# Kernel tuning notes

Measured on AMD Instinct MI355X. Metric: run time of the kernel, lower is better.

The kernel has to match this reference:

```python
import jax, jax.numpy as jnp
import numpy as np

EMBED = 1024
HEADS = 16
INTERNAL = 1024  # embedding_dim // downsample_rate
HEAD_DIM = INTERNAL // HEADS


def setup_inputs() -> dict:
    key = jax.random.key(0)
    ks = jax.random.split(key, 12)
    B, S = 2, 2048
    s_in = 1.0 / np.sqrt(EMBED)
    s_out = 1.0 / np.sqrt(INTERNAL)
    return {
        "queries": jax.random.normal(ks[0], (B, S, EMBED), jnp.float32),
        "keys": jax.random.normal(ks[1], (B, S, EMBED), jnp.float32),
        "values": jax.random.normal(ks[2], (B, S, EMBED), jnp.float32),
        "Wq": jax.random.uniform(ks[3], (EMBED, INTERNAL), jnp.float32, -s_in, s_in),
        "bq": jax.random.uniform(ks[4], (INTERNAL,), jnp.float32, -s_in, s_in),
        "Wk": jax.random.uniform(ks[5], (EMBED, INTERNAL), jnp.float32, -s_in, s_in),
        "bk": jax.random.uniform(ks[6], (INTERNAL,), jnp.float32, -s_in, s_in),
        "Wv": jax.random.uniform(ks[7], (EMBED, INTERNAL), jnp.float32, -s_in, s_in),
        "bv": jax.random.uniform(ks[8], (INTERNAL,), jnp.float32, -s_in, s_in),
        "Wo": jax.random.uniform(ks[9], (INTERNAL, EMBED), jnp.float32, -s_out, s_out),
        "bo": jax.random.uniform(ks[10], (EMBED,), jnp.float32, -s_out, s_out),
    }


def _split_heads(x):
    B, S, D = x.shape
    return x.reshape(B, S, HEADS, D // HEADS).transpose(0, 2, 1, 3)  # bhsd


def reference(queries, keys, values, Wq, bq, Wk, bk, Wv, bv, Wo, bo):
    q = _split_heads(queries @ Wq + bq)
    k = _split_heads(keys @ Wk + bk)
    v = _split_heads(values @ Wv + bv)
    # NOTE: original scales by 1/sqrt(internal_dim), not 1/sqrt(head_dim)
    scale = 1.0 / np.sqrt(INTERNAL).astype(np.float32)
    scores = jnp.einsum("bhqd,bhkd->bhqk", q, k) * scale
    probs = jax.nn.softmax(scores, axis=-1)
    out = jnp.einsum("bhqk,bhkd->bhqd", probs, v)
    B, H, S, Dh = out.shape
    out = out.transpose(0, 2, 1, 3).reshape(B, S, H * Dh)
    return out @ Wo + bo
```

## Files before the change

kernel.cpp:

```cpp
#include <hip/hip_runtime.h>
#include <stdint.h>

typedef unsigned short u16;
typedef __attribute__((ext_vector_type(8))) short short8;
typedef __attribute__((ext_vector_type(4))) float f32x4;
typedef __attribute__((ext_vector_type(16))) float f32x16;
typedef __attribute__((ext_vector_type(8))) unsigned short u16x8;
typedef __attribute__((ext_vector_type(4))) unsigned short u16x4;
typedef __attribute__((ext_vector_type(4))) uint32_t u32x4;

#if __has_builtin(__builtin_amdgcn_exp2f)
#define EXP2(x) __builtin_amdgcn_exp2f(x)
#else
#define EXP2(x) exp2f(x)
#endif

__device__ __forceinline__ u16 f2bf(float f) {
  union { float f; uint32_t u; } v; v.f = f;
  uint32_t r = (v.u + 0x7FFFu + ((v.u >> 16) & 1u)) >> 16;
  return (u16)r;
}

__device__ __forceinline__ uint32_t pack2(float a, float b) {
  return (__float_as_uint(b) & 0xffff0000u) | (__float_as_uint(a) >> 16);
}

__device__ __forceinline__ void gload_lds16(const void* g, void* l) {
  __builtin_amdgcn_global_load_lds(
      (const __attribute__((address_space(1))) void*)g,
      (__attribute__((address_space(3))) void*)l,
      16, 0, 0);
}

__global__ __launch_bounds__(256) void cvt_x(const float* __restrict__ q,
                                             const float* __restrict__ k,
                                             const float* __restrict__ v,
                                             u16* __restrict__ dst) {
  const float* src = blockIdx.z == 0 ? q : (blockIdx.z == 1 ? k : v);
  u16* d = dst + (size_t)blockIdx.z * (4096u * 1024u);
  size_t i = ((size_t)blockIdx.x * 256 + threadIdx.x) * 8;
  float4 a = *(const float4*)(src + i);
  float4 b = *(const float4*)(src + i + 4);
  u16x8 o;
  o[0] = f2bf(a.x); o[1] = f2bf(a.y); o[2] = f2bf(a.z); o[3] = f2bf(a.w);
  o[4] = f2bf(b.x); o[5] = f2bf(b.y); o[6] = f2bf(b.z); o[7] = f2bf(b.w);
  *(u16x8*)(d + i) = o;
}

__global__ __launch_bounds__(256) void cvt_wt(const float* __restrict__ Wq,
                                              const float* __restrict__ Wk,
                                              const float* __restrict__ Wv,
                                              const float* __restrict__ Wo,
                                              u16* __restrict__ Wt4) {
  const float* W = blockIdx.z == 0 ? Wq : (blockIdx.z == 1 ? Wk
                   : (blockIdx.z == 2 ? Wv : Wo));
  u16* Wt = Wt4 + (size_t)blockIdx.z * (1024u * 1024u);
  __shared__ u16 tile[64][65];
  int kt = blockIdx.x * 64, nt = blockIdx.y * 64;
  int t = threadIdx.x;
#pragma unroll
  for (int r = 0; r < 4; ++r) {
    int id = t + r * 256;
    int kk = id >> 4, c4 = id & 15;
    float4 vv = *(const float4*)(W + (size_t)(kt + kk) * 1024 + nt + c4 * 4);
    tile[kk][c4 * 4 + 0] = f2bf(vv.x);
    tile[kk][c4 * 4 + 1] = f2bf(vv.y);
    tile[kk][c4 * 4 + 2] = f2bf(vv.z);
    tile[kk][c4 * 4 + 3] = f2bf(vv.w);
  }
  __syncthreads();
#pragma unroll
  for (int r = 0; r < 4; ++r) {
    int id = t + r * 256;
    int n = id >> 4, kc = id & 15;
    u16x4 o;
    o[0] = tile[kc * 4 + 0][n];
    o[1] = tile[kc * 4 + 1][n];
    o[2] = tile[kc * 4 + 2][n];
    o[3] = tile[kc * 4 + 3][n];
    *(u16x4*)(Wt + (size_t)(nt + n) * 1024 + kt + kc * 4) = o;
  }
}

template <bool F32OUT>
__device__ __forceinline__ void gemm_tile(const u16* __restrict__ A,
                                          const u16* __restrict__ Bt,
                                          const float* __restrict__ bias,
                                          u16* __restrict__ Cb,
                                          float* __restrict__ Cf,
                                          float scale, int bm, int bn) {
  __shared__ u16 Alds[128 * 64];
  __shared__ u16 Blds[128 * 64];
  const int tid = threadIdx.x;
  const int lane = tid & 63, w = tid >> 6;
  const int wm = (w >> 1) * 64, wn = (w & 1) * 64;
  const int l15 = lane & 15, lg = lane >> 4;

  f32x4 acc[4][4] = {};

  int srow[4], scol[4], soff[4];
#pragma unroll
  for (int i = 0; i < 4; ++i) {
    int o = (w * 4 + i) * 1024 + lane * 16;
    int row = o >> 7;
    int kc = ((o >> 4) & 7) ^ (row & 7);
    srow[i] = row; scol[i] = kc * 8; soff[i] = o;
  }

  for (int kt = 0; kt < 16; ++kt) {
    __syncthreads();
#pragma unroll
    for (int i = 0; i < 4; ++i) {
      gload_lds16(A + (size_t)(bm * 128 + srow[i]) * 1024 + kt * 64 + scol[i],
                  (char*)Alds + soff[i]);
      gload_lds16(Bt + (size_t)(bn * 128 + srow[i]) * 1024 + kt * 64 + scol[i],
                  (char*)Blds + soff[i]);
    }
    __syncthreads();
#pragma unroll
    for (int ks = 0; ks < 2; ++ks) {
      short8 af[4], bf[4];
#pragma unroll
      for (int m = 0; m < 4; ++m) {
        int r = wm + m * 16 + l15;
        int byt = r * 128 + ((ks * 64 + lg * 16) ^ ((r & 7) << 4));
        af[m] = *(const short8*)((const char*)Alds + byt);
      }
#pragma unroll
      for (int n = 0; n < 4; ++n) {
        int r = wn + n * 16 + l15;
        int byt = r * 128 + ((ks * 64 + lg * 16) ^ ((r & 7) << 4));
        bf[n] = *(const short8*)((const char*)Blds + byt);
      }
#pragma unroll
      for (int m = 0; m < 4; ++m)
#pragma unroll
        for (int n = 0; n < 4; ++n)
          acc[m][n] = __builtin_amdgcn_mfma_f32_16x16x32_bf16(
              af[m], bf[n], acc[m][n], 0, 0, 0);
    }
  }
#pragma unroll
  for (int m = 0; m < 4; ++m) {
    int row0 = bm * 128 + wm + m * 16 + lg * 4;
#pragma unroll
    for (int n = 0; n < 4; ++n) {
      int col = bn * 128 + wn + n * 16 + l15;
      float bvv = bias[col];
#pragma unroll
      for (int r = 0; r < 4; ++r) {
        float v = (acc[m][n][r] + bvv) * scale;
        if (F32OUT)
          Cf[(size_t)(row0 + r) * 1024 + col] = v;
        else
          Cb[(size_t)(row0 + r) * 1024 + col] = f2bf(v);
      }
    }
  }
}

__global__ __launch_bounds__(256) void proj_kernel(const u16* __restrict__ X3,
                                                   const u16* __restrict__ Wt3,
                                                   const float* __restrict__ bq,
                                                   const float* __restrict__ bk,
                                                   const float* __restrict__ bv,
                                                   u16* __restrict__ out3) {
  int z = blockIdx.z;
  const float* bias = z == 0 ? bq : (z == 1 ? bk : bv);
  float scale = z == 0 ? 0.045084220f : 1.0f;
  gemm_tile<false>(X3 + (size_t)z * 4096 * 1024, Wt3 + (size_t)z * 1024 * 1024,
                   bias, out3 + (size_t)z * 4096 * 1024, nullptr, scale,
                   blockIdx.x, blockIdx.y);
}

__global__ __launch_bounds__(256) void outproj_kernel(const u16* __restrict__ Att,
                                                      const u16* __restrict__ Wot,
                                                      const float* __restrict__ bo,
                                                      float* __restrict__ out) {
  gemm_tile<true>(Att, Wot, bo, nullptr, out, 1.0f, blockIdx.x, blockIdx.y);
}

__global__ __launch_bounds__(256) void vt_kernel(const u16* __restrict__ v,
                                                 u16* __restrict__ vt) {
  int bh = blockIdx.y;
  int sbase = blockIdx.x * 64;
  int b = bh >> 4, h = bh & 15;
  __shared__ u16 tile[64][65];
  int t = threadIdx.x;
#pragma unroll
  for (int r = 0; r < 2; ++r) {
    int id = t + r * 256;
    int s = id >> 3, dc = id & 7;
    u16x8 x = *(const u16x8*)(v + (size_t)(b * 2048 + sbase + s) * 1024 +
                              h * 64 + dc * 8);
#pragma unroll
    for (int j = 0; j < 8; ++j) tile[s][dc * 8 + j] = x[j];
  }
  __syncthreads();
#pragma unroll
  for (int r = 0; r < 2; ++r) {
    int id = t + r * 256;
    int d = id >> 3, sc = id & 7;
    u16x8 o;
#pragma unroll
    for (int j = 0; j < 8; ++j) o[j] = tile[sc * 8 + j][d];
    *(u16x8*)(vt + ((size_t)bh * 64 + d) * 2048 + sbase + sc * 8) = o;
  }
}

__global__ __launch_bounds__(256) void attn_kernel(const u16* __restrict__ q,
                                                   const u16* __restrict__ k,
                                                   const u16* __restrict__ vt,
                                                   u16* __restrict__ att) {
  __shared__ u16 smem[8192];
  const int tid = threadIdx.x, lane = tid & 63, w = tid >> 6;
  const int l31 = lane & 31, hi = lane >> 5;
  const int bh = blockIdx.y, b = bh >> 4, h = bh & 15;
  const int qb = blockIdx.x * 128 + w * 32;

  short8 qf[4];
  const u16* qrow = q + (size_t)(b * 2048 + qb + l31) * 1024 + h * 64 + hi * 8;
#pragma unroll
  for (int s = 0; s < 4; ++s) qf[s] = *(const short8*)(qrow + s * 16);

  f32x16 acc0 = {}, acc1 = {};
  float lsum = 0.f;

  int soff[2], krow[2], vrow[2], scol[2];
#pragma unroll
  for (int i = 0; i < 2; ++i) {
    int o = i * 4096 + tid * 16;
    int row = o >> 7;
    int kc = ((o >> 4) & 7) ^ (row & 7);
    soff[i] = o; scol[i] = kc * 8; vrow[i] = row;
    krow[i] = row ^ (((((row >> 2) ^ (row >> 3)) & 1)) ? 12 : 0);
  }
  const u16* ksrc = k + (size_t)b * 2048 * 1024 + h * 64;
  const u16* vsrc = vt + (size_t)bh * 64 * 2048;
  const char* KL = (const char*)smem;
  const char* VL = (const char*)smem + 8192;

  for (int t = 0; t < 32; ++t) {
    const int kbase = t * 64;
    __syncthreads();
#pragma unroll
    for (int i = 0; i < 2; ++i) {
      gload_lds16(ksrc + (size_t)(kbase + krow[i]) * 1024 + scol[i],
                  (char*)smem + soff[i]);
      gload_lds16(vsrc + (size_t)vrow[i] * 2048 + kbase + scol[i],
                  (char*)smem + 8192 + soff[i]);
    }
    __syncthreads();

#pragma unroll
    for (int kg = 0; kg < 2; ++kg) {
      f32x16 sc = {};
#pragma unroll
      for (int s = 0; s < 4; ++s) {
        int row = kg * 32 + l31;
        int byt = row * 128 + ((s * 32 + hi * 16) ^ ((row & 7) << 4));
        short8 ak = *(const short8*)(KL + byt);
        sc = __builtin_amdgcn_mfma_f32_32x32x16_bf16(ak, qf[s], sc, 0, 0, 0);
      }
      float p[16];
#pragma unroll
      for (int g = 0; g < 16; ++g) p[g] = EXP2(sc[g]);
#pragma unroll
      for (int g = 0; g < 16; g += 4)
        lsum += (p[g] + p[g + 1]) + (p[g + 2] + p[g + 3]);
#pragma unroll
      for (int c = 0; c < 2; ++c) {
        u32x4 fw;
        fw[0] = pack2(p[8 * c + 0], p[8 * c + 1]);
        fw[1] = pack2(p[8 * c + 2], p[8 * c + 3]);
        fw[2] = pack2(p[8 * c + 4], p[8 * c + 5]);
        fw[3] = pack2(p[8 * c + 6], p[8 * c + 7]);
        short8 pf = __builtin_bit_cast(short8, fw);
        int colv = kg * 64 + c * 32 + hi * 16;
        {
          int byt = l31 * 128 + (colv ^ ((l31 & 7) << 4));
          short8 bv_ = *(const short8*)(VL + byt);
          acc0 = __builtin_amdgcn_mfma_f32_32x32x16_bf16(pf, bv_, acc0, 0, 0, 0);
        }
        {
          int r1 = 32 + l31;
          int byt = r1 * 128 + (colv ^ ((r1 & 7) << 4));
          short8 bv_ = *(const short8*)(VL + byt);
          acc1 = __builtin_amdgcn_mfma_f32_32x32x16_bf16(pf, bv_, acc1, 0, 0, 0);
        }
      }
    }
  }

  float ltot = lsum + __shfl_xor(lsum, 32);
  float rinv = 1.0f / ltot;
  __syncthreads();
  u16* tw = smem + w * 2048;
#pragma unroll
  for (int r = 0; r < 16; ++r) {
    int row = (r & 3) + 8 * (r >> 2) + 4 * hi;
    float ri = __shfl(rinv, row);
    tw[row * 64 + l31] = (u16)(__float_as_uint(acc0[r] * ri) >> 16);
    tw[row * 64 + 32 + l31] = (u16)(__float_as_uint(acc1[r] * ri) >> 16);
  }
  asm volatile("s_waitcnt lgkmcnt(0)" ::: "memory");
  __builtin_amdgcn_sched_barrier(0);
  u16* abase = att + (size_t)(b * 2048 + qb) * 1024 + h * 64;
#pragma unroll
  for (int i = 0; i < 4; ++i) {
    int id = lane + i * 64;
    int row = id >> 3, ch = id & 7;
    u16x8 vv = *(const u16x8*)(tw + row * 64 + ch * 8);
    *(u16x8*)(abase + (size_t)row * 1024 + ch * 8) = vv;
  }
}

extern "C" void kernel_launch(void* const* d_in, const int* in_sizes, int n_in,
                              void* d_out, int out_size, void* d_ws,
                              size_t ws_size, hipStream_t stream) {
  const float* Q  = (const float*)d_in[0];
  const float* K  = (const float*)d_in[1];
  const float* V  = (const float*)d_in[2];
  const float* Wq = (const float*)d_in[3];
  const float* bq = (const float*)d_in[4];
  const float* Wk = (const float*)d_in[5];
  const float* bk = (const float*)d_in[6];
  const float* Wv = (const float*)d_in[7];
  const float* bv = (const float*)d_in[8];
  const float* Wo = (const float*)d_in[9];
  const float* bo = (const float*)d_in[10];
  float* out = (float*)d_out;

  u16* ws = (u16*)d_ws;
  const size_t SZX = (size_t)4096 * 1024;
  const size_t SZW = (size_t)1024 * 1024;
  u16* Xbf   = ws;
  u16* Wtbf  = ws + 3 * SZX;
  u16* QKVbf = Wtbf + 4 * SZW;
  u16* VTbf  = QKVbf + 3 * SZX;
  u16* ATTbf = VTbf + SZX;

  hipLaunchKernelGGL(cvt_x, dim3(2048, 1, 3), dim3(256), 0, stream, Q, K, V,
                     Xbf);
  hipLaunchKernelGGL(cvt_wt, dim3(16, 16, 4), dim3(256), 0, stream, Wq, Wk, Wv,
                     Wo, Wtbf);
  hipLaunchKernelGGL(proj_kernel, dim3(32, 8, 3), dim3(256), 0, stream, Xbf,
                     Wtbf, bq, bk, bv, QKVbf);
  hipLaunchKernelGGL(vt_kernel, dim3(32, 32), dim3(256), 0, stream,
                     QKVbf + 2 * SZX, VTbf);
  hipLaunchKernelGGL(attn_kernel, dim3(16, 32), dim3(256), 0, stream, QKVbf,
                     QKVbf + SZX, VTbf, ATTbf);
  hipLaunchKernelGGL(outproj_kernel, dim3(32, 8), dim3(256), 0, stream, ATTbf,
                     Wtbf + 3 * SZW, bo, out);
}
```

Baseline: 132.2 us.

## Double-buffer K/V tiles and process two query groups per wave in attention

```diff
diff --git a/kernel.cpp b/kernel.cpp
--- a/kernel.cpp
+++ b/kernel.cpp
@@ -208,106 +208,132 @@
   }
 }
 
-__global__ __launch_bounds__(256) void attn_kernel(const u16* __restrict__ q,
-                                                   const u16* __restrict__ k,
-                                                   const u16* __restrict__ vt,
-                                                   u16* __restrict__ att) {
-  __shared__ u16 smem[8192];
+__global__ __launch_bounds__(256, 1) void attn_kernel(const u16* __restrict__ q,
+                                                      const u16* __restrict__ k,
+                                                      const u16* __restrict__ vt,
+                                                      u16* __restrict__ att) {
+  __shared__ u16 smem[16384];
   const int tid = threadIdx.x, lane = tid & 63, w = tid >> 6;
   const int l31 = lane & 31, hi = lane >> 5;
   const int bh = blockIdx.y, b = bh >> 4, h = bh & 15;
-  const int qb = blockIdx.x * 128 + w * 32;
-
-  short8 qf[4];
-  const u16* qrow = q + (size_t)(b * 2048 + qb + l31) * 1024 + h * 64 + hi * 8;
-#pragma unroll
-  for (int s = 0; s < 4; ++s) qf[s] = *(const short8*)(qrow + s * 16);
-
-  f32x16 acc0 = {}, acc1 = {};
-  float lsum = 0.f;
-
-  int soff[2], krow[2], vrow[2], scol[2];
+  const int qb = blockIdx.x * 256 + w * 64;
+
+  short8 qf[2][4];
+#pragma unroll
+  for (int g = 0; g < 2; ++g) {
+    const u16* qrow =
+        q + (size_t)(b * 2048 + qb + g * 32 + l31) * 1024 + h * 64 + hi * 8;
+#pragma unroll
+    for (int s = 0; s < 4; ++s) qf[g][s] = *(const short8*)(qrow + s * 16);
+  }
+
+  f32x16 acc[2][2] = {};
+  float lsum[2] = {0.f, 0.f};
+
+  int scol[2], rowK[2], rowV[2];
 #pragma unroll
   for (int i = 0; i < 2; ++i) {
-    int o = i * 4096 + tid * 16;
-    int row = o >> 7;
-    int kc = ((o >> 4) & 7) ^ (row & 7);
-    soff[i] = o; scol[i] = kc * 8; vrow[i] = row;
-    krow[i] = row ^ (((((row >> 2) ^ (row >> 3)) & 1)) ? 12 : 0);
+    int gi = i * 256 + tid;
+    int row = gi & 63, c16 = gi >> 6;
+    scol[i] = c16 * 8;
+    rowV[i] = row;
+    rowK[i] = row ^ ((((row >> 2) ^ (row >> 3)) & 1) ? 12 : 0);
   }
   const u16* ksrc = k + (size_t)b * 2048 * 1024 + h * 64;
   const u16* vsrc = vt + (size_t)bh * 64 * 2048;
-  const char* KL = (const char*)smem;
-  const char* VL = (const char*)smem + 8192;
+
+#pragma unroll
+  for (int i = 0; i < 2; ++i) {
+    gload_lds16(ksrc + (size_t)rowK[i] * 1024 + scol[i],
+                (char*)smem + i * 4096 + tid * 16);
+    gload_lds16(vsrc + (size_t)rowV[i] * 2048 + scol[i],
+                (char*)smem + 8192 + i * 4096 + tid * 16);
+  }
 
   for (int t = 0; t < 32; ++t) {
-    const int kbase = t * 64;
+    const int cur = t & 1;
     __syncthreads();
-#pragma unroll
-    for (int i = 0; i < 2; ++i) {
-      gload_lds16(ksrc + (size_t)(kbase + krow[i]) * 1024 + scol[i],
-                  (char*)smem + soff[i]);
-      gload_lds16(vsrc + (size_t)vrow[i] * 2048 + kbase + scol[i],
-                  (char*)smem + 8192 + soff[i]);
-    }
-    __syncthreads();
+    if (t + 1 < 32) {
+      char* dst = (char*)smem + (cur ^ 1) * 16384;
+      const int kb2 = (t + 1) * 64;
+#pragma unroll
+      for (int i = 0; i < 2; ++i) {
+        gload_lds16(ksrc + (size_t)(kb2 + rowK[i]) * 1024 + scol[i],
+                    dst + i * 4096 + tid * 16);
+        gload_lds16(vsrc + (size_t)rowV[i] * 2048 + kb2 + scol[i],
+                    dst + 8192 + i * 4096 + tid * 16);
+      }
+    }
+    const char* KL = (const char*)smem + cur * 16384;
+    const char* VL = KL + 8192;
 
 #pragma unroll
     for (int kg = 0; kg < 2; ++kg) {
-      f32x16 sc = {};
-#pragma unroll
-      for (int s = 0; s < 4; ++s) {
-        int row = kg * 32 + l31;
-        int byt = row * 128 + ((s * 32 + hi * 16) ^ ((row & 7) << 4));
-        short8 ak = *(const short8*)(KL + byt);
-        sc = __builtin_amdgcn_mfma_f32_32x32x16_bf16(ak, qf[s], sc, 0, 0, 0);
-      }
-      float p[16];
-#pragma unroll
-      for (int g = 0; g < 16; ++g) p[g] = EXP2(sc[g]);
-#pragma unroll
-      for (int g = 0; g < 16; g += 4)
-        lsum += (p[g] + p[g + 1]) + (p[g + 2] + p[g + 3]);
-#pragma unroll
-      for (int c = 0; c < 2; ++c) {
-        u32x4 fw;
-        fw[0] = pack2(p[8 * c + 0], p[8 * c + 1]);
-        fw[1] = pack2(p[8 * c + 2], p[8 * c + 3]);
-        fw[2] = pack2(p[8 * c + 4], p[8 * c + 5]);
-        fw[3] = pack2(p[8 * c + 6], p[8 * c + 7]);
-        short8 pf = __builtin_bit_cast(short8, fw);
-        int colv = kg * 64 + c * 32 + hi * 16;
-        {
-          int byt = l31 * 128 + (colv ^ ((l31 & 7) << 4));
-          short8 bv_ = *(const short8*)(VL + byt);
-          acc0 = __builtin_amdgcn_mfma_f32_32x32x16_bf16(pf, bv_, acc0, 0, 0, 0);
+      short8 ak[4], bv[4];
+#pragma unroll
+      for (int s = 0; s < 4; ++s)
+        ak[s] = *(const short8*)(KL + (s * 2 + hi) * 1024 +
+                                 (kg * 32 + l31) * 16);
+#pragma unroll
+      for (int c = 0; c < 2; ++c)
+#pragma unroll
+        for (int half = 0; half < 2; ++half)
+          bv[c * 2 + half] =
+              *(const short8*)(VL + (kg * 4 + c * 2 + hi) * 1024 +
+                               (half * 32 + l31) * 16);
+#pragma unroll
+      for (int g = 0; g < 2; ++g) {
+        f32x16 sc = {};
+#pragma unroll
+        for (int s = 0; s < 4; ++s)
+          sc = __builtin_amdgcn_mfma_f32_32x32x16_bf16(ak[s], qf[g][s], sc,
+                                                       0, 0, 0);
+        float p[16];
+#pragma unroll
+        for (int e = 0; e < 16; ++e) p[e] = EXP2(sc[e]);
+#pragma unroll
+        for (int e = 0; e < 16; e += 4)
+          lsum[g] += (p[e] + p[e + 1]) + (p[e + 2] + p[e + 3]);
+#pragma unroll
+        for (int c = 0; c < 2; ++c) {
+          u32x4 fw;
+          fw[0] = pack2(p[8 * c + 0], p[8 * c + 1]);
+          fw[1] = pack2(p[8 * c + 2], p[8 * c + 3]);
+          fw[2] = pack2(p[8 * c + 4], p[8 * c + 5]);
+          fw[3] = pack2(p[8 * c + 6], p[8 * c + 7]);
+          short8 pf = __builtin_bit_cast(short8, fw);
+          acc[g][0] = __builtin_amdgcn_mfma_f32_32x32x16_bf16(
+              pf, bv[c * 2 + 0], acc[g][0], 0, 0, 0);
+          acc[g][1] = __builtin_amdgcn_mfma_f32_32x32x16_bf16(
+              pf, bv[c * 2 + 1], acc[g][1], 0, 0, 0);
         }
-        {
-          int r1 = 32 + l31;
-          int byt = r1 * 128 + (colv ^ ((r1 & 7) << 4));
-          short8 bv_ = *(const short8*)(VL + byt);
-          acc1 = __builtin_amdgcn_mfma_f32_32x32x16_bf16(pf, bv_, acc1, 0, 0, 0);
-        }
-      }
-    }
-  }
-
-  float ltot = lsum + __shfl_xor(lsum, 32);
-  float rinv = 1.0f / ltot;
+      }
+    }
+  }
+
+  float rinv[2];
+#pragma unroll
+  for (int g = 0; g < 2; ++g) {
+    float ltot = lsum[g] + __shfl_xor(lsum[g], 32);
+    rinv[g] = 1.0f / ltot;
+  }
   __syncthreads();
-  u16* tw = smem + w * 2048;
-#pragma unroll
-  for (int r = 0; r < 16; ++r) {
-    int row = (r & 3) + 8 * (r >> 2) + 4 * hi;
-    float ri = __shfl(rinv, row);
-    tw[row * 64 + l31] = (u16)(__float_as_uint(acc0[r] * ri) >> 16);
-    tw[row * 64 + 32 + l31] = (u16)(__float_as_uint(acc1[r] * ri) >> 16);
-  }
+  u16* tw = smem + w * 4096;
+#pragma unroll
+  for (int g = 0; g < 2; ++g)
+#pragma unroll
+    for (int r = 0; r < 16; ++r) {
+      int rq = (r & 3) + 8 * (r >> 2) + 4 * hi;
+      float ri = __shfl(rinv[g], rq);
+      int row = g * 32 + rq;
+      tw[row * 64 + l31] = (u16)(__float_as_uint(acc[g][0][r] * ri) >> 16);
+      tw[row * 64 + 32 + l31] = (u16)(__float_as_uint(acc[g][1][r] * ri) >> 16);
+    }
   asm volatile("s_waitcnt lgkmcnt(0)" ::: "memory");
   __builtin_amdgcn_sched_barrier(0);
   u16* abase = att + (size_t)(b * 2048 + qb) * 1024 + h * 64;
 #pragma unroll
-  for (int i = 0; i < 4; ++i) {
+  for (int i = 0; i < 8; ++i) {
     int id = lane + i * 64;
     int row = id >> 3, ch = id & 7;
     u16x8 vv = *(const u16x8*)(tw + row * 64 + ch * 8);
@@ -348,7 +374,7 @@
                      Wtbf, bq, bk, bv, QKVbf);
   hipLaunchKernelGGL(vt_kernel, dim3(32, 32), dim3(256), 0, stream,
                      QKVbf + 2 * SZX, VTbf);
-  hipLaunchKernelGGL(attn_kernel, dim3(16, 32), dim3(256), 0, stream, QKVbf,
+  hipLaunchKernelGGL(attn_kernel, dim3(8, 32), dim3(256), 0, stream, QKVbf,
                      QKVbf + SZX, VTbf, ATTbf);
   hipLaunchKernelGGL(outproj_kernel, dim3(32, 8), dim3(256), 0, stream, ATTbf,
                      Wtbf + 3 * SZW, bo, out);
```

New measurement: 126.9 us. 4.0% less time.
